# Kernel tuning notes

Hardware: AMD Instinct MI355X
Metric: run time of the kernel (lower is better)

The kernel has to match this reference:

```python
import jax, jax.numpy as jnp
import numpy as np

SIZE = 8192
DIM = 256
N = 32768
BETA = 0.25
DECAY = 0.99
EPS = 1e-5


def setup_inputs() -> dict:
    key = jax.random.key(0)
    kz, ke = jax.random.split(key)
    z = jax.random.normal(kz, (N, DIM), dtype=jnp.float32)
    # init = randn * 0.1, ema_embed_sum initialized as a clone of embeddings
    embeddings = jax.random.normal(ke, (SIZE, DIM), dtype=jnp.float32) * 0.1
    ema_embed_sum = embeddings
    ema_cluster_size = jnp.zeros((SIZE,), dtype=jnp.float32)
    usage_counter = jnp.zeros((SIZE,), dtype=jnp.int64)
    return {
        "z": z,
        "embeddings": embeddings,
        "ema_cluster_size": ema_cluster_size,
        "ema_embed_sum": ema_embed_sum,
        "usage_counter": usage_counter,
    }


def reference(z, embeddings, ema_cluster_size, ema_embed_sum, usage_counter):
    # Squared euclidean distances; argmin is identical to cdist argmin.
    z2 = jnp.sum(z * z, axis=-1, keepdims=True)              # [N, 1]
    e2 = jnp.sum(embeddings * embeddings, axis=-1)           # [K]
    d2 = z2 - 2.0 * jnp.matmul(z, embeddings.T) + e2         # [N, K]
    indices = jnp.argmin(d2, axis=-1)                         # [N]

    quantized = embeddings[indices]                           # [N, D] gather

    # usage_counter: vectorized equivalent of the per-index python loop
    counts_f = jax.ops.segment_sum(
        jnp.ones((z.shape[0],), dtype=jnp.float32), indices, num_segments=SIZE
    )                                                         # [K] == onehot.sum(0)
    new_usage = usage_counter + counts_f.astype(usage_counter.dtype)

    sg = jax.lax.stop_gradient
    commit_loss = BETA * jnp.mean((z - sg(quantized)) ** 2)
    codebook_loss = jnp.mean((quantized - sg(z)) ** 2)
    loss = commit_loss + codebook_loss

    # EMA update (training mode), all under no-grad semantics
    embed_sum = jax.ops.segment_sum(z, indices, num_segments=SIZE)  # onehot.T @ z
    new_cluster_size = DECAY * ema_cluster_size + (1.0 - DECAY) * counts_f
    new_embed_sum = DECAY * ema_embed_sum + (1.0 - DECAY) * embed_sum
    n = jnp.sum(new_cluster_size)
    cluster = (new_cluster_size + EPS) / (n + SIZE * EPS) * n
    new_embeddings = new_embed_sum / cluster[:, None]

    # straight-through estimator
    quantized_st = z + sg(quantized - z)
    return (indices, quantized_st, loss, new_embeddings, new_cluster_size,
            new_embed_sum, new_usage)
```

## Files before the change

kernel.cpp:

```cpp
#include <hip/hip_runtime.h>

#define NZ 32768
#define KE 8192
#define DD 256
#define NCHUNK 4
#define CH (KE / NCHUNK)
#define NSLICE (NCHUNK * 4)
#define ITERS ((CH / 128) * 8)
#define THR_GAP 0.05f
#define BIASF 128.0f

typedef __attribute__((ext_vector_type(8))) _Float16 f16x8;
typedef __attribute__((ext_vector_type(4))) float f32x4;
typedef unsigned int uint32;


__device__ __forceinline__ float wave_reduce_sum(float v) {
#pragma unroll
  for (int m = 32; m >= 1; m >>= 1) v += __shfl_xor(v, m, 64);
  return v;
}

__global__ void prep_kernel(const float* __restrict__ emb, unsigned short* __restrict__ e_dst,
                            float* __restrict__ e_sq, const float* __restrict__ z,
                            unsigned short* __restrict__ z_dst, float* __restrict__ z_sq,
                            const float* __restrict__ ema_cs, float* __restrict__ sema_out,
                            float* __restrict__ o_loss) {
  const int gb = blockIdx.x;
  if (gb < (KE / 4) + (NZ / 4)) {
    const float* src;
    unsigned short* dst;
    float* sq;
    int row;
    if (gb < KE / 4) {
      src = emb; dst = e_dst; sq = e_sq;
      row = gb * 4 + (threadIdx.x >> 6);
    } else {
      src = z; dst = z_dst; sq = z_sq;
      row = (gb - KE / 4) * 4 + (threadIdx.x >> 6);
    }
    const int lane = threadIdx.x & 63;
    const float4 v = *reinterpret_cast<const float4*>(src + (size_t)row * DD + lane * 4);
    alignas(8) _Float16 hv[4] = {(_Float16)v.x, (_Float16)v.y, (_Float16)v.z, (_Float16)v.w};
    *reinterpret_cast<uint2*>(dst + (size_t)row * DD + lane * 4) =
        *reinterpret_cast<const uint2*>(hv);
    float s = (v.x * v.x + v.y * v.y) + (v.z * v.z + v.w * v.w);
    s = wave_reduce_sum(s);
    if (lane == 0) sq[row] = s;
  } else {
    __shared__ float red[256];
    float s = 0.f;
    for (int i = threadIdx.x; i < KE; i += 256) s += ema_cs[i];
    red[threadIdx.x] = s;
    __syncthreads();
    for (int off = 128; off >= 1; off >>= 1) {
      if (threadIdx.x < off) red[threadIdx.x] += red[threadIdx.x + off];
      __syncthreads();
    }
    if (threadIdx.x == 0) {
      sema_out[0] = red[0];
      o_loss[0] = 0.f;
    }
  }
}


#define LSTR 32

#define LDSA(ki, r) (&ldsB[ki][r][0])

#define LOADB(RS, itv)                                                          \
  if ((itv) < ITERS) {                                                          \
    const int kb_ = ((itv) & 7) * 32;                                           \
    const size_t bo_ = (size_t)((itv) >> 3) * 128 * DD + kb_;                   \
    RS##b0 = *reinterpret_cast<const uint4*>(ef + boff0 + bo_);                 \
  }

#define WRITEB(buf, RS)                                                         \
  *reinterpret_cast<uint4*>(&ldsB[buf][ur][usw]) = RS##b0;

__launch_bounds__(512, 1)
__global__ void mfma_argmin_kernel(const unsigned short* __restrict__ zf,
                                   const unsigned short* __restrict__ ef,
                                   const float* __restrict__ e2,
                                   float4* __restrict__ pt) {
  __shared__ unsigned short ldsB[8][128][LSTR];
  const int bid = blockIdx.x;
  const int c = (bid & 7) >> 1;
  const int mblk = ((bid >> 3) << 1) | (bid & 1);
  const int row0 = mblk * 128;
  const int cbase = c * CH;
  const int tid = threadIdx.x;
  const int wid = tid >> 6, lane = tid & 63;
  const int wr = wid >> 2, wc = wid & 3;
  const int lg = lane >> 4, l15 = lane & 15;

  const int ur = tid >> 2;
  const int usw = (((tid & 3) ^ ((ur >> 1) & 3)) << 3);
  const int csw = ((lg ^ ((l15 >> 1) & 3)) << 3);
  const size_t aoff0 = (size_t)(row0 + ur) * DD + (tid & 3) * 8;
  const size_t boff0 = (size_t)(cbase + ur) * DD + (tid & 3) * 8;

  uint32 k1[4][4], k2[4][4];
#pragma unroll
  for (int i = 0; i < 4; ++i)
#pragma unroll
    for (int r = 0; r < 4; ++r) { k1[i][r] = 0xFFFFFFFFu; k2[i][r] = 0xFFFFFFFFu; }

  f32x4 acc[4][2];
  f16x8 areg[8][4];

  uint4 q0_b0, q1_b0, q2_b0, q3_b0;

  LOADB(q0_, 0)
  LOADB(q1_, 1)
  LOADB(q2_, 2)
  LOADB(q3_, 3)
#pragma unroll
  for (int ki = 0; ki < 8; ++ki) {
    const uint4 va0 = *reinterpret_cast<const uint4*>(zf + aoff0 + ki * 32);
    *reinterpret_cast<uint4*>(LDSA(ki, ur) + usw) = va0;
  }
  __syncthreads();
#pragma unroll
  for (int ki = 0; ki < 8; ++ki)
#pragma unroll
    for (int x = 0; x < 4; ++x)
      areg[ki][x] =
          *reinterpret_cast<const f16x8*>(LDSA(ki, wr * 64 + x * 16 + l15) + csw);
  __syncthreads();
  WRITEB(0, q0_)
  WRITEB(1, q1_)
  WRITEB(2, q2_)
  WRITEB(3, q3_)
  LOADB(q0_, 4)
  LOADB(q1_, 5)
  LOADB(q2_, 6)
  LOADB(q3_, 7)
  __syncthreads();

#define COMPUTE(buf, itv)                                                               \
  {                                                                                     \
    const int ki_ = (itv) & 7;                                                          \
    if (ki_ == 0) {                                                                     \
      _Pragma("unroll") for (int i = 0; i < 4; ++i)                                     \
          _Pragma("unroll") for (int j = 0; j < 2; ++j) acc[i][j] = (f32x4)(0.f);       \
    }                                                                                   \
    f16x8 bh[2];                                                                        \
    _Pragma("unroll") for (int x = 0; x < 2; ++x)                                       \
      bh[x] = *reinterpret_cast<const f16x8*>(&ldsB[buf][wc * 32 + x * 16 + l15][csw]); \
    _Pragma("unroll") for (int i = 0; i < 4; ++i)                                       \
        _Pragma("unroll") for (int j = 0; j < 2; ++j)                                   \
            acc[i][j] = __builtin_amdgcn_mfma_f32_16x16x32_f16(areg[ki_][i], bh[j], acc[i][j], 0, 0, 0); \
    if (ki_ == 7) {                                                                     \
      const int col0 = cbase + ((itv) >> 3) * 128;                                      \
      const uint32 tb_ = (uint32)(((itv) >> 3) << 2);                                   \
      _Pragma("unroll") for (int j = 0; j < 2; ++j) {                                   \
        const int code = col0 + wc * 32 + j * 16 + l15;                                 \
        const float e2b = e2[code] + BIASF;                                             \
        const uint32 meta = tb_ | (uint32)j;                                            \
        _Pragma("unroll") for (int i = 0; i < 4; ++i)                                   \
            _Pragma("unroll") for (int r = 0; r < 4; ++r) {                             \
          const float vb = fmaf(-2.f, acc[i][j][r], e2b);                               \
          const uint32 key = (__float_as_uint(vb) & 0xFFFFFFC0u) | meta;                \
          const uint32 hi = max(k1[i][r], key);                                         \
          k1[i][r] = min(k1[i][r], key);                                                \
          k2[i][r] = min(k2[i][r], hi);                                                 \
        }                                                                               \
      }                                                                                 \
    }                                                                                   \
  }

  for (int it = 0; it < ITERS; it += 8) {
    WRITEB(4, q0_)
    LOADB(q0_, it + 8)
    COMPUTE(0, it)
    WRITEB(5, q1_)
    LOADB(q1_, it + 9)
    COMPUTE(1, it + 1)
    WRITEB(6, q2_)
    LOADB(q2_, it + 10)
    COMPUTE(2, it + 2)
    WRITEB(7, q3_)
    LOADB(q3_, it + 11)
    COMPUTE(3, it + 3)
    __syncthreads();
    WRITEB(0, q0_)
    LOADB(q0_, it + 12)
    COMPUTE(4, it + 4)
    WRITEB(1, q1_)
    LOADB(q1_, it + 13)
    COMPUTE(5, it + 5)
    WRITEB(2, q2_)
    LOADB(q2_, it + 14)
    COMPUTE(6, it + 6)
    WRITEB(3, q3_)
    LOADB(q3_, it + 15)
    COMPUTE(7, it + 7)
    __syncthreads();
  }

  float bv1[4][4], bv2[4][4];
  uint32 bpi[4][4];
  const uint32 cb_ = (uint32)(cbase + wc * 32 + l15);
#pragma unroll
  for (int i = 0; i < 4; ++i)
#pragma unroll
    for (int r = 0; r < 4; ++r) {
      const uint32 a1 = k1[i][r], a2 = k2[i][r];
      bv1[i][r] = __uint_as_float(a1 & 0xFFFFFFC0u) - BIASF;
      bv2[i][r] = __uint_as_float(a2 & 0xFFFFFFC0u) - BIASF;
      const uint32 c1 = cb_ + ((a1 & 60u) >> 2) * 128u + ((a1 & 3u) << 4);
      const uint32 c2 = cb_ + ((a2 & 60u) >> 2) * 128u + ((a2 & 3u) << 4);
      bpi[i][r] = c1 | (c2 << 16);
    }

#pragma unroll
  for (int m = 1; m <= 8; m <<= 1) {
#pragma unroll
    for (int i = 0; i < 4; ++i)
#pragma unroll
      for (int r = 0; r < 4; ++r) {
        const float ov1 = __shfl_xor(bv1[i][r], m, 64);
        const float ov2 = __shfl_xor(bv2[i][r], m, 64);
        const uint32 op = (uint32)__shfl_xor((int)bpi[i][r], m, 64);
        const uint32 ai1 = bpi[i][r] & 0xFFFFu, oi1 = op & 0xFFFFu;
        const bool ol = (ov1 < bv1[i][r]) || (ov1 == bv1[i][r] && oi1 < ai1);
        const float w1 = ol ? ov1 : bv1[i][r];
        const uint32 wi1 = ol ? oi1 : ai1;
        const float w2 = ol ? ov2 : bv2[i][r];
        const uint32 wi2 = ol ? (op >> 16) : (bpi[i][r] >> 16);
        const float l1 = ol ? bv1[i][r] : ov1;
        const uint32 li1 = ol ? ai1 : oi1;
        const bool s2 = (l1 < w2) || (l1 == w2 && li1 < wi2);
        bv1[i][r] = w1;
        bv2[i][r] = s2 ? l1 : w2;
        bpi[i][r] = wi1 | ((s2 ? li1 : wi2) << 16);
      }
  }
  if (l15 == 0) {
    const int slice = c * 4 + wc;
#pragma unroll
    for (int i = 0; i < 4; ++i)
#pragma unroll
      for (int r = 0; r < 4; ++r) {
        const int row = row0 + wr * 64 + i * 16 + lg * 4 + r;
        pt[(size_t)slice * NZ + row] =
            make_float4(bv1[i][r], bv2[i][r], __uint_as_float(bpi[i][r]), 0.f);
      }
  }
}

__global__ void combine_kernel(const float* __restrict__ z, const float* __restrict__ emb,
                               const float* __restrict__ z2, const float* __restrict__ e2,
                               const float4* __restrict__ pt, float* __restrict__ oidx_f,
                               int* __restrict__ oidx_i, float* __restrict__ oq,
                               float* __restrict__ oloss) {
  const int row = blockIdx.x * 4 + (threadIdx.x >> 6);
  const int lane = threadIdx.x & 63;
  const int wid = threadIdx.x >> 6;
  const float4 p = pt[(size_t)(lane & 15) * NZ + row];
  const float v1 = p.x, v2 = p.y;
  const uint32 pk = __float_as_uint(p.z);
  float m = v1;
#pragma unroll
  for (int s = 1; s <= 8; s <<= 1) m = fminf(m, __shfl_xor(m, s, 64));

  const float4 zv = *reinterpret_cast<const float4*>(z + (size_t)row * DD + lane * 4);
  const float z2r = z2[row];
  float bestd = 3.4e38f;
  int besti = KE;
#pragma unroll 1
  for (int cnum = 0; cnum < 32; ++cnum) {
    const int src = (lane & 48) | (cnum >> 1);
    const float vc = __shfl((cnum & 1) ? v2 : v1, src, 64);
    const uint32 pkc = (uint32)__shfl((int)pk, src, 64);
    const int idxc = (cnum & 1) ? (int)(pkc >> 16) : (int)(pkc & 0xFFFFu);
    if (vc < m + THR_GAP) {
      const float4 ev = *reinterpret_cast<const float4*>(emb + (size_t)idxc * DD + lane * 4);
      float s = (zv.x * ev.x + zv.y * ev.y) + (zv.z * ev.z + zv.w * ev.w);
      s = wave_reduce_sum(s);
      const float d = (z2r - 2.f * s) + e2[idxc];
      if (d < bestd || (d == bestd && idxc < besti)) { bestd = d; besti = idxc; }
    }
  }
  if (lane == 0) {
    oidx_f[row] = (float)besti;
    oidx_i[row] = besti;
  }
  const float4 qv = *reinterpret_cast<const float4*>(emb + (size_t)besti * DD + lane * 4);
  *reinterpret_cast<float4*>(oq + (size_t)row * DD + lane * 4) = qv;
  const float dx = zv.x - qv.x, dy = zv.y - qv.y, dz = zv.z - qv.z, dw = zv.w - qv.w;
  float s = (dx * dx + dy * dy) + (dz * dz + dw * dw);
  s = wave_reduce_sum(s);
  __shared__ float red[4];
  if (lane == 0) red[wid] = s;
  __syncthreads();
  if (threadIdx.x == 0) {
    const float t = (red[0] + red[1]) + (red[2] + red[3]);
    atomicAdd(oloss, t * (1.25f / ((float)NZ * (float)DD)));
  }
}

__global__ void perk_kernel(const float* __restrict__ z, const float* __restrict__ ema_cs,
                            const float* __restrict__ ema_es, const int* __restrict__ usage,
                            const int* __restrict__ idx, const float* __restrict__ sema,
                            float* __restrict__ o_emb, float* __restrict__ o_cs,
                            float* __restrict__ o_es, float* __restrict__ o_us) {
  const int k0 = blockIdx.x * 8;
  const int tid = threadIdx.x;
  __shared__ int cnt;
  __shared__ int cnt8[8];
  __shared__ int stot[8];
  __shared__ int rows[2048];
  float acc[8];
#pragma unroll
  for (int q = 0; q < 8; ++q) acc[q] = 0.f;
  if (tid < 8) stot[tid] = 0;
  for (int base = 0; base < NZ; base += 2048) {
    if (tid == 0) cnt = 0;
    if (tid < 8) cnt8[tid] = 0;
    __syncthreads();
#pragma unroll
    for (int t = 0; t < 2048; t += 256) {
      const int r = base + t + tid;
      const int q = idx[r] - k0;
      if ((unsigned)q < 8u) {
        rows[atomicAdd(&cnt, 1)] = (r << 3) | q;
        atomicAdd(&cnt8[q], 1);
      }
    }
    __syncthreads();
    const int cq = cnt;
    if (tid < 8) stot[tid] += cnt8[tid];
    for (int m = 0; m < cq; ++m) {
      const int rr = rows[m];
      const float v = z[(size_t)(rr >> 3) * DD + tid];
      const int q = rr & 7;
#pragma unroll
      for (int qq = 0; qq < 8; ++qq)
        if (qq == q) acc[qq] += v;
    }
    __syncthreads();
  }
  const float n = 0.99f * sema[0] + 0.01f * (float)NZ;
  const float dn = n + (float)KE * 1e-5f;
#pragma unroll
  for (int q = 0; q < 8; ++q) {
    const float ncs = 0.99f * ema_cs[k0 + q] + 0.01f * (float)stot[q];
    const float nes = 0.99f * ema_es[(size_t)(k0 + q) * DD + tid] + 0.01f * acc[q];
    o_es[(size_t)(k0 + q) * DD + tid] = nes;
    o_emb[(size_t)(k0 + q) * DD + tid] = nes / ((ncs + 1e-5f) / dn * n);
  }
  if (tid < 8) {
    o_cs[k0 + tid] = 0.99f * ema_cs[k0 + tid] + 0.01f * (float)stot[tid];
    o_us[k0 + tid] = (float)(usage[k0 + tid] + stot[tid]);
  }
}


extern "C" void kernel_launch(void* const* d_in, const int* in_sizes, int n_in,
                              void* d_out, int out_size, void* d_ws, size_t ws_size,
                              hipStream_t stream) {
  const float* z = (const float*)d_in[0];
  const float* emb = (const float*)d_in[1];
  const float* ema_cs = (const float*)d_in[2];
  const float* ema_es = (const float*)d_in[3];
  const int* usage = (const int*)d_in[4];

  float* out = (float*)d_out;
  float* o_idx = out;
  float* o_q = o_idx + NZ;
  float* o_loss = o_q + (size_t)NZ * DD;
  float* o_emb = o_loss + 1;
  float* o_cs = o_emb + (size_t)KE * DD;
  float* o_es = o_cs + KE;
  float* o_us = o_es + (size_t)KE * DD;

  char* w = (char*)d_ws;
  size_t off = 0;
  auto alloc = [&](size_t bytes) -> char* {
    char* r = w + off;
    off = (off + bytes + 255) & ~(size_t)255;
    return r;
  };
  float* ws_e2 = (float*)alloc(KE * 4);
  float* ws_z2 = (float*)alloc(NZ * 4);
  float* ws_sema = (float*)alloc(256);
  int* ws_idx = (int*)alloc(NZ * 4);
  float4* ws_pt = (float4*)alloc((size_t)NSLICE * NZ * 16);
  unsigned short* z_f16 = (unsigned short*)alloc((size_t)NZ * DD * 2);
  unsigned short* e_f16 = (unsigned short*)alloc((size_t)KE * DD * 2);
  (void)ws_size;

  prep_kernel<<<(KE / 4) + (NZ / 4) + 1, 256, 0, stream>>>(emb, e_f16, ws_e2, z, z_f16,
                                                           ws_z2, ema_cs, ws_sema, o_loss);

  mfma_argmin_kernel<<<(NZ / 128) * NCHUNK, 512, 0, stream>>>(z_f16, e_f16, ws_e2, ws_pt);
  combine_kernel<<<NZ / 4, 256, 0, stream>>>(z, emb, ws_z2, ws_e2, ws_pt, o_idx, ws_idx,
                                             o_q, o_loss);
  perk_kernel<<<KE / 8, 256, 0, stream>>>(z, ema_cs, ema_es, usage, ws_idx, ws_sema,
                                          o_emb, o_cs, o_es, o_us);
}
```

Baseline: 361.3 us.

## Stage codebook tiles with direct global-to-LDS loads and cache e2 in LDS

```diff
diff --git a/kernel.cpp b/kernel.cpp
--- a/kernel.cpp
+++ b/kernel.cpp
@@ -69,15 +69,14 @@
 
 #define LDSA(ki, r) (&ldsB[ki][r][0])
 
-#define LOADB(RS, itv)                                                          \
+#define STAGEB(buf, itv)                                                        \
   if ((itv) < ITERS) {                                                          \
     const int kb_ = ((itv) & 7) * 32;                                           \
     const size_t bo_ = (size_t)((itv) >> 3) * 128 * DD + kb_;                   \
-    RS##b0 = *reinterpret_cast<const uint4*>(ef + boff0 + bo_);                 \
-  }
-
-#define WRITEB(buf, RS)                                                         \
-  *reinterpret_cast<uint4*>(&ldsB[buf][ur][usw]) = RS##b0;
+    __builtin_amdgcn_global_load_lds(                                           \
+        (const uint32*)(ef + bsw + bo_), (uint32*)&ldsB[buf][wid * 16][0],      \
+        16, 0, 0);                                                              \
+  }
 
 __launch_bounds__(512, 1)
 __global__ void mfma_argmin_kernel(const unsigned short* __restrict__ zf,
@@ -85,6 +84,7 @@
                                    const float* __restrict__ e2,
                                    float4* __restrict__ pt) {
   __shared__ unsigned short ldsB[8][128][LSTR];
+  __shared__ float ldsE2[CH];
   const int bid = blockIdx.x;
   const int c = (bid & 7) >> 1;
   const int mblk = ((bid >> 3) << 1) | (bid & 1);
@@ -99,7 +99,7 @@
   const int usw = (((tid & 3) ^ ((ur >> 1) & 3)) << 3);
   const int csw = ((lg ^ ((l15 >> 1) & 3)) << 3);
   const size_t aoff0 = (size_t)(row0 + ur) * DD + (tid & 3) * 8;
-  const size_t boff0 = (size_t)(cbase + ur) * DD + (tid & 3) * 8;
+  const size_t bsw = (size_t)(cbase + ur) * DD + ((lane & 3) ^ ((lane >> 3) & 3)) * 8;
 
   uint32 k1[4][4], k2[4][4];
 #pragma unroll
@@ -110,12 +110,7 @@
   f32x4 acc[4][2];
   f16x8 areg[8][4];
 
-  uint4 q0_b0, q1_b0, q2_b0, q3_b0;
-
-  LOADB(q0_, 0)
-  LOADB(q1_, 1)
-  LOADB(q2_, 2)
-  LOADB(q3_, 3)
+  for (int i = tid; i < CH; i += 512) ldsE2[i] = e2[cbase + i] + BIASF;
 #pragma unroll
   for (int ki = 0; ki < 8; ++ki) {
     const uint4 va0 = *reinterpret_cast<const uint4*>(zf + aoff0 + ki * 32);
@@ -129,14 +124,10 @@
       areg[ki][x] =
           *reinterpret_cast<const f16x8*>(LDSA(ki, wr * 64 + x * 16 + l15) + csw);
   __syncthreads();
-  WRITEB(0, q0_)
-  WRITEB(1, q1_)
-  WRITEB(2, q2_)
-  WRITEB(3, q3_)
-  LOADB(q0_, 4)
-  LOADB(q1_, 5)
-  LOADB(q2_, 6)
-  LOADB(q3_, 7)
+  STAGEB(0, 0)
+  STAGEB(1, 1)
+  STAGEB(2, 2)
+  STAGEB(3, 3)
   __syncthreads();
 
 #define COMPUTE(buf, itv)                                                               \
@@ -153,11 +144,10 @@
         _Pragma("unroll") for (int j = 0; j < 2; ++j)                                   \
             acc[i][j] = __builtin_amdgcn_mfma_f32_16x16x32_f16(areg[ki_][i], bh[j], acc[i][j], 0, 0, 0); \
     if (ki_ == 7) {                                                                     \
-      const int col0 = cbase + ((itv) >> 3) * 128;                                      \
+      const int e2o = (((itv) >> 3) << 7) + wc * 32 + l15;                              \
       const uint32 tb_ = (uint32)(((itv) >> 3) << 2);                                   \
       _Pragma("unroll") for (int j = 0; j < 2; ++j) {                                   \
-        const int code = col0 + wc * 32 + j * 16 + l15;                                 \
-        const float e2b = e2[code] + BIASF;                                             \
+        const float e2b = ldsE2[e2o + j * 16];                                          \
         const uint32 meta = tb_ | (uint32)j;                                            \
         _Pragma("unroll") for (int i = 0; i < 4; ++i)                                   \
             _Pragma("unroll") for (int r = 0; r < 4; ++r) {                             \
@@ -172,30 +162,22 @@
   }
 
   for (int it = 0; it < ITERS; it += 8) {
-    WRITEB(4, q0_)
-    LOADB(q0_, it + 8)
+    STAGEB(4, it + 4)
+    STAGEB(5, it + 5)
+    STAGEB(6, it + 6)
+    STAGEB(7, it + 7)
     COMPUTE(0, it)
-    WRITEB(5, q1_)
-    LOADB(q1_, it + 9)
     COMPUTE(1, it + 1)
-    WRITEB(6, q2_)
-    LOADB(q2_, it + 10)
     COMPUTE(2, it + 2)
-    WRITEB(7, q3_)
-    LOADB(q3_, it + 11)
     COMPUTE(3, it + 3)
     __syncthreads();
-    WRITEB(0, q0_)
-    LOADB(q0_, it + 12)
+    STAGEB(0, it + 8)
+    STAGEB(1, it + 9)
+    STAGEB(2, it + 10)
+    STAGEB(3, it + 11)
     COMPUTE(4, it + 4)
-    WRITEB(1, q1_)
-    LOADB(q1_, it + 13)
     COMPUTE(5, it + 5)
-    WRITEB(2, q2_)
-    LOADB(q2_, it + 14)
     COMPUTE(6, it + 6)
-    WRITEB(3, q3_)
-    LOADB(q3_, it + 15)
     COMPUTE(7, it + 7)
     __syncthreads();
   }
```

After: 365.7 us. Within noise of the previous version (+1.2%).
